# Optimization experiments

Measured on AMD Instinct MI355X. Metric: run time of the kernel, lower is better.

## Reference

```python
import jax, jax.numpy as jnp
import numpy as np

N_NODES = 50000
N_EDGES = 600000
DIN, DH, DOUT = 128, 256, 128
BN_EPS = 1e-5
LRELU_SLOPE = 0.01


def setup_inputs() -> dict:
    key = jax.random.key(0)
    ks = jax.random.split(key, 16)
    rn = lambda k, s, sc=0.05: jax.random.normal(k, s, dtype=jnp.float32) * sc
    return {
        'nodes': jax.random.normal(ks[0], (N_NODES, DIN), dtype=jnp.float32),
        'src': jax.random.randint(ks[1], (N_EDGES,), 0, N_NODES, dtype=jnp.int32),
        'dst': jax.random.randint(ks[2], (N_EDGES,), 0, N_NODES, dtype=jnp.int32),
        # FeedForward params
        'Wf1': rn(ks[3], (DIN, DH)), 'bf1': jnp.zeros((DH,), jnp.float32),
        'gf1': jnp.ones((DH,), jnp.float32), 'bef1': jnp.zeros((DH,), jnp.float32),
        'Wf2': rn(ks[4], (DH, DIN)), 'bf2': jnp.zeros((DIN,), jnp.float32),
        'gf2': jnp.ones((DIN,), jnp.float32), 'bef2': jnp.zeros((DIN,), jnp.float32),
        # SAGEConv 1 (in->hidden)
        'Ws1': rn(ks[5], (DIN, DH)), 'Wn1': rn(ks[6], (DIN, DH)), 'b1': jnp.zeros((DH,), jnp.float32),
        'gs1': jnp.ones((DH,), jnp.float32), 'bs1': jnp.zeros((DH,), jnp.float32),
        # SAGEConv 2 (hidden->out)
        'Ws2': rn(ks[7], (DH, DOUT)), 'Wn2': rn(ks[8], (DH, DOUT)), 'b2': jnp.zeros((DOUT,), jnp.float32),
        'gs2': jnp.ones((DOUT,), jnp.float32), 'bs2': jnp.zeros((DOUT,), jnp.float32),
    }


def _bn(x, gamma, beta):
    # BatchNorm1d, training mode: batch stats over node dim, biased variance
    mu = jnp.mean(x, axis=0)
    var = jnp.mean(jnp.square(x - mu), axis=0)
    return (x - mu) * jax.lax.rsqrt(var + BN_EPS) * gamma + beta


def _sage_mean(x, src, dst, Wself, Wneigh, bias):
    # DGL SAGEConv('mean'): out = x@Wself + mean_{src->dst}(x[src])@Wneigh + bias
    n = x.shape[0]
    deg = jax.ops.segment_sum(jnp.ones_like(src, dtype=x.dtype), dst, num_segments=n)
    agg = jax.ops.segment_sum(x[src], dst, num_segments=n)  # [N, d] irregular scatter-add
    h_neigh = agg / jnp.maximum(deg, 1.0)[:, None]
    return x @ Wself + h_neigh @ Wneigh + bias


def reference(nodes, src, dst, Wf1, bf1, gf1, bef1, Wf2, bf2, gf2, bef2,
              Ws1, Wn1, b1, gs1, bs1, Ws2, Wn2, b2, gs2, bs2):
    # FeedForward (dropout=0 -> identity)
    h = jax.nn.relu(_bn(nodes @ Wf1 + bf1, gf1, bef1))
    h = jax.nn.relu(_bn(h @ Wf2 + bf2, gf2, bef2))
    # SAGE layer 1
    h1 = _sage_mean(h, src, dst, Ws1, Wn1, b1)
    h1 = jax.nn.leaky_relu(_bn(h1, gs1, bs1), LRELU_SLOPE)
    # SAGE layer 2
    h2 = _sage_mean(h1, src, dst, Ws2, Wn2, b2)
    return jax.nn.leaky_relu(_bn(h2, gs2, bs2), LRELU_SLOPE)
```

## Files before the change

### kernel.cpp

```cpp
#include <hip/hip_runtime.h>

#define DIN 128
#define BN_EPS 1e-5f

typedef __attribute__((ext_vector_type(8))) short bf16x8;
typedef __attribute__((ext_vector_type(4))) float f32x4;
typedef unsigned int u32;

__device__ __forceinline__ ushort f2bf(float f) {
    unsigned u = __float_as_uint(f);
    u += 0x7fffu + ((u >> 16) & 1u);
    return (ushort)(u >> 16);
}
__device__ __forceinline__ float bf2f(ushort h) {
    return __uint_as_float(((unsigned)h) << 16);
}

template<int KC, int STATS>
__global__ __launch_bounds__(256) void gemm_wreg(
    const ushort* __restrict__ A, const ushort* __restrict__ BT,
    ushort* __restrict__ C, int mStrips, int N, int K, int logNG,
    float* __restrict__ gsums, float* __restrict__ gsqs)
{
    int tid = threadIdx.x;
    int lane = tid & 63;
    int gw = blockIdx.x * 4 + (tid >> 6);
    int wg = gw & ((1 << logNG) - 1);
    int set = gw >> logNG;
    int totalSets = (gridDim.x * 4) >> logNG;
    int cl = lane & 15, q = lane >> 4;
    int colBase = wg * 64;

    bf16x8 bf[4][KC];
    #pragma unroll
    for (int nt = 0; nt < 4; nt++) {
        const ushort* bp = BT + (long)(colBase + nt * 16 + cl) * K + q * 8;
        #pragma unroll
        for (int kc = 0; kc < KC; kc++)
            bf[nt][kc] = *(const bf16x8*)(bp + kc * 32);
    }

    float ssum[4] = {0.f, 0.f, 0.f, 0.f};
    float ssq[4]  = {0.f, 0.f, 0.f, 0.f};

    for (int strip = set; strip < mStrips; strip += totalSets) {
        int rowBase = strip * 16;
        const ushort* ap = A + (long)(rowBase + cl) * K + q * 8;
        bf16x8 af[KC];
        #pragma unroll
        for (int kc = 0; kc < KC; kc++)
            af[kc] = *(const bf16x8*)(ap + kc * 32);
        f32x4 acc[4] = {};
        #pragma unroll
        for (int kc = 0; kc < KC; kc++)
            #pragma unroll
            for (int nt = 0; nt < 4; nt++)
                acc[nt] = __builtin_amdgcn_mfma_f32_16x16x32_bf16(af[kc], bf[nt][kc], acc[nt], 0, 0, 0);
        #pragma unroll
        for (int nt = 0; nt < 4; nt++) {
            #pragma unroll
            for (int r = 0; r < 4; r++) {
                float v = acc[nt][r];
                long row = rowBase + q * 4 + r;
                C[row * N + colBase + nt * 16 + cl] = f2bf(v);
                if (STATS) { ssum[nt] += v; ssq[nt] += v * v; }
            }
        }
    }

    if (STATS) {
        #pragma unroll
        for (int nt = 0; nt < 4; nt++) {
            ssum[nt] += __shfl_xor(ssum[nt], 16, 64);
            ssum[nt] += __shfl_xor(ssum[nt], 32, 64);
            ssq[nt]  += __shfl_xor(ssq[nt], 16, 64);
            ssq[nt]  += __shfl_xor(ssq[nt], 32, 64);
        }
        if (q == 0) {
            #pragma unroll
            for (int nt = 0; nt < 4; nt++) {
                atomicAdd(&gsums[colBase + nt * 16 + cl], ssum[nt]);
                atomicAdd(&gsqs[colBase + nt * 16 + cl], ssq[nt]);
            }
        }
    }
}

__global__ void bnparam_kernel(const float* __restrict__ sums, const float* __restrict__ sqs,
                               const float* __restrict__ gamma, const float* __restrict__ beta,
                               float* __restrict__ scale, float* __restrict__ shift,
                               int N, float invM)
{
    int c = blockIdx.x * blockDim.x + threadIdx.x;
    if (c < N) {
        float mean = sums[c] * invM;
        float var = sqs[c] * invM - mean * mean;
        float sc = gamma[c] * rsqrtf(var + BN_EPS);
        scale[c] = sc;
        shift[c] = beta[c] - mean * sc;
    }
}

__global__ __launch_bounds__(256) void bnact_bf16(
    const ushort* __restrict__ X, const float* __restrict__ scale, const float* __restrict__ shift,
    ushort* __restrict__ O, int total4, int logN, int outStride, float negSlope)
{
    int stride = gridDim.x * blockDim.x;
    int Nm1 = (1 << logN) - 1;
    for (int t = blockIdx.x * blockDim.x + threadIdx.x; t < total4; t += stride) {
        int idx = t * 4;
        int row = idx >> logN;
        int c = idx & Nm1;
        ushort4 v4 = *(const ushort4*)&X[idx];
        float4 sc = *(const float4*)&scale[c];
        float4 sh = *(const float4*)&shift[c];
        float a = bf2f(v4.x) * sc.x + sh.x; a = (a > 0.f) ? a : a * negSlope;
        float b = bf2f(v4.y) * sc.y + sh.y; b = (b > 0.f) ? b : b * negSlope;
        float d = bf2f(v4.z) * sc.z + sh.z; d = (d > 0.f) ? d : d * negSlope;
        float e = bf2f(v4.w) * sc.w + sh.w; e = (e > 0.f) ? e : e * negSlope;
        ushort4 o; o.x = f2bf(a); o.y = f2bf(b); o.z = f2bf(d); o.w = f2bf(e);
        *(ushort4*)&O[(long)row * outStride + c] = o;
    }
}

__global__ __launch_bounds__(256) void bnact_f32(
    float* __restrict__ X, const float* __restrict__ scale, const float* __restrict__ shift,
    int total4, int logN, float negSlope)
{
    int stride = gridDim.x * blockDim.x;
    int Nm1 = (1 << logN) - 1;
    for (int t = blockIdx.x * blockDim.x + threadIdx.x; t < total4; t += stride) {
        int idx = t * 4;
        int c = idx & Nm1;
        float4 v = *(const float4*)&X[idx];
        float4 sc = *(const float4*)&scale[c];
        float4 sh = *(const float4*)&shift[c];
        float a = v.x * sc.x + sh.x; a = (a > 0.f) ? a : a * negSlope;
        float b = v.y * sc.y + sh.y; b = (b > 0.f) ? b : b * negSlope;
        float d = v.z * sc.z + sh.z; d = (d > 0.f) ? d : d * negSlope;
        float e = v.w * sc.w + sh.w; e = (e > 0.f) ? e : e * negSlope;
        *(float4*)&X[idx] = make_float4(a, b, d, e);
    }
}

__global__ __launch_bounds__(256) void colstats128(
    const float* __restrict__ X, float* __restrict__ sums, float* __restrict__ sqs, int M)
{
    __shared__ float ss[128], sq[128];
    int tid = threadIdx.x;
    if (tid < 128) { ss[tid] = 0.f; sq[tid] = 0.f; }
    __syncthreads();
    int cg = tid & 31;
    int worker = (blockIdx.x << 3) | (tid >> 5);
    int totalW = gridDim.x << 3;
    float4 s4 = make_float4(0, 0, 0, 0), q4 = make_float4(0, 0, 0, 0);
    for (int r = worker; r < M; r += totalW) {
        float4 v = *(const float4*)&X[(long)r * 128 + cg * 4];
        s4.x += v.x; s4.y += v.y; s4.z += v.z; s4.w += v.w;
        q4.x += v.x * v.x; q4.y += v.y * v.y; q4.z += v.z * v.z; q4.w += v.w * v.w;
    }
    atomicAdd(&ss[cg * 4 + 0], s4.x); atomicAdd(&sq[cg * 4 + 0], q4.x);
    atomicAdd(&ss[cg * 4 + 1], s4.y); atomicAdd(&sq[cg * 4 + 1], q4.y);
    atomicAdd(&ss[cg * 4 + 2], s4.z); atomicAdd(&sq[cg * 4 + 2], q4.z);
    atomicAdd(&ss[cg * 4 + 3], s4.w); atomicAdd(&sq[cg * 4 + 3], q4.w);
    __syncthreads();
    if (tid < 128) { atomicAdd(&sums[tid], ss[tid]); atomicAdd(&sqs[tid], sq[tid]); }
}

__global__ void convert_nodes(const float* __restrict__ X, ushort* __restrict__ O, int total4)
{
    int t = blockIdx.x * blockDim.x + threadIdx.x;
    if (t < total4) {
        float4 v = *(const float4*)&X[t * 4];
        ushort4 o; o.x = f2bf(v.x); o.y = f2bf(v.y); o.z = f2bf(v.z); o.w = f2bf(v.w);
        *(ushort4*)&O[t * 4] = o;
    }
}

__global__ void wt_all(const float* __restrict__ W0, const float* __restrict__ W1,
                       const float* __restrict__ W2, const float* __restrict__ W3,
                       const float* __restrict__ W4, const float* __restrict__ W5,
                       ushort* __restrict__ WT)
{
    int seg = blockIdx.y;
    const float* W; int logK, dstBase, stride, kOff;
    switch (seg) {
        case 0: W = W0; logK = 7; dstBase = 0;      stride = 128; kOff = 0;   break;
        case 1: W = W1; logK = 8; dstBase = 32768;  stride = 256; kOff = 0;   break;
        case 2: W = W2; logK = 7; dstBase = 65536;  stride = 256; kOff = 0;   break;
        case 3: W = W3; logK = 7; dstBase = 65536;  stride = 256; kOff = 128; break;
        case 4: W = W4; logK = 8; dstBase = 131072; stride = 256; kOff = 0;   break;
        default:W = W5; logK = 8; dstBase = 163840; stride = 256; kOff = 0;   break;
    }
    int t = blockIdx.x * blockDim.x + threadIdx.x;
    int N = 32768 >> logK;
    int k = t & ((1 << logK) - 1);
    int n = t >> logK;
    WT[(long)dstBase + (long)n * stride + kOff + k] = f2bf(W[(long)k * N + n]);
}

__global__ void degcount_kernel(const int* __restrict__ dst, int* __restrict__ degi, int E)
{
    int i = blockIdx.x * blockDim.x + threadIdx.x;
    if (i < E) atomicAdd(&degi[dst[i]], 1);
}

__global__ __launch_bounds__(256) void scan_block_sums(const int* __restrict__ degi,
                                                       int* __restrict__ partial, int n)
{
    __shared__ int s[256];
    int i = blockIdx.x * 256 + threadIdx.x;
    s[threadIdx.x] = (i < n) ? degi[i] : 0;
    __syncthreads();
    for (int off = 128; off > 0; off >>= 1) {
        if (threadIdx.x < off) s[threadIdx.x] += s[threadIdx.x + off];
        __syncthreads();
    }
    if (threadIdx.x == 0) partial[blockIdx.x] = s[0];
}

__global__ __launch_bounds__(256) void scan_partials(int* __restrict__ partial, int nb)
{
    __shared__ int s[256];
    int v = (threadIdx.x < nb) ? partial[threadIdx.x] : 0;
    s[threadIdx.x] = v;
    __syncthreads();
    for (int off = 1; off < 256; off <<= 1) {
        int t = (threadIdx.x >= off) ? s[threadIdx.x - off] : 0;
        __syncthreads();
        s[threadIdx.x] += t;
        __syncthreads();
    }
    if (threadIdx.x < nb) partial[threadIdx.x] = s[threadIdx.x] - v;
}

__global__ __launch_bounds__(256) void scan_final(const int* __restrict__ degi,
                                                  const int* __restrict__ partial,
                                                  int* __restrict__ rowstart, int n)
{
    __shared__ int s[256];
    int i = blockIdx.x * 256 + threadIdx.x;
    int v = (i < n) ? degi[i] : 0;
    s[threadIdx.x] = v;
    __syncthreads();
    for (int off = 1; off < 256; off <<= 1) {
        int t = (threadIdx.x >= off) ? s[threadIdx.x - off] : 0;
        __syncthreads();
        s[threadIdx.x] += t;
        __syncthreads();
    }
    if (i < n) rowstart[i] = partial[blockIdx.x] + s[threadIdx.x] - v;
}

__global__ void fillcsr_kernel(const int* __restrict__ src, const int* __restrict__ dst,
                               const int* __restrict__ rowstart, int* __restrict__ cursor,
                               int* __restrict__ csr, int E)
{
    int i = blockIdx.x * blockDim.x + threadIdx.x;
    if (i < E) {
        int d = dst[i];
        int p = atomicAdd(&cursor[d], 1);
        csr[rowstart[d] + p] = src[i];
    }
}

__global__ __launch_bounds__(256) void gather_bf(
    const ushort* __restrict__ X, const int* __restrict__ rowstart,
    const int* __restrict__ degi, const int* __restrict__ csr,
    ushort* __restrict__ O, int nN)
{
    int wv = (blockIdx.x * blockDim.x + threadIdx.x) >> 6;
    int lane = threadIdx.x & 63;
    if (wv >= nN) return;
    int start = rowstart[wv], d = degi[wv];
    float a0 = 0.f, a1 = 0.f;
    int col = lane * 2;
    int j = 0;
    for (; j + 4 <= d; j += 4) {
        int s0 = csr[start + j + 0];
        int s1 = csr[start + j + 1];
        int s2 = csr[start + j + 2];
        int s3 = csr[start + j + 3];
        unsigned p0 = *(const unsigned*)(X + (long)s0 * 256 + col);
        unsigned p1 = *(const unsigned*)(X + (long)s1 * 256 + col);
        unsigned p2 = *(const unsigned*)(X + (long)s2 * 256 + col);
        unsigned p3 = *(const unsigned*)(X + (long)s3 * 256 + col);
        a0 += bf2f((ushort)(p0 & 0xffff)) + bf2f((ushort)(p1 & 0xffff))
            + bf2f((ushort)(p2 & 0xffff)) + bf2f((ushort)(p3 & 0xffff));
        a1 += bf2f((ushort)(p0 >> 16)) + bf2f((ushort)(p1 >> 16))
            + bf2f((ushort)(p2 >> 16)) + bf2f((ushort)(p3 >> 16));
    }
    for (; j < d; j++) {
        int s0 = csr[start + j];
        unsigned p0 = *(const unsigned*)(X + (long)s0 * 256 + col);
        a0 += bf2f((ushort)(p0 & 0xffff));
        a1 += bf2f((ushort)(p0 >> 16));
    }
    float inv = 1.f / fmaxf((float)d, 1.f);
    unsigned o = (unsigned)f2bf(a0 * inv) | ((unsigned)f2bf(a1 * inv) << 16);
    *(unsigned*)(O + (long)wv * 256 + col) = o;
}

__global__ __launch_bounds__(256) void gather_fuse(
    const ushort* __restrict__ Z, const int* __restrict__ rowstart,
    const int* __restrict__ degi, const int* __restrict__ csr,
    float* __restrict__ O, int nN)
{
    int wv = (blockIdx.x * blockDim.x + threadIdx.x) >> 6;
    int lane = threadIdx.x & 63;
    if (wv >= nN) return;
    int start = rowstart[wv], d = degi[wv];
    float a0 = 0.f, a1 = 0.f;
    int col = lane * 2;
    int j = 0;
    for (; j + 4 <= d; j += 4) {
        int s0 = csr[start + j + 0];
        int s1 = csr[start + j + 1];
        int s2 = csr[start + j + 2];
        int s3 = csr[start + j + 3];
        unsigned p0 = *(const unsigned*)(Z + (long)s0 * 256 + col);
        unsigned p1 = *(const unsigned*)(Z + (long)s1 * 256 + col);
        unsigned p2 = *(const unsigned*)(Z + (long)s2 * 256 + col);
        unsigned p3 = *(const unsigned*)(Z + (long)s3 * 256 + col);
        a0 += bf2f((ushort)(p0 & 0xffff)) + bf2f((ushort)(p1 & 0xffff))
            + bf2f((ushort)(p2 & 0xffff)) + bf2f((ushort)(p3 & 0xffff));
        a1 += bf2f((ushort)(p0 >> 16)) + bf2f((ushort)(p1 >> 16))
            + bf2f((ushort)(p2 >> 16)) + bf2f((ushort)(p3 >> 16));
    }
    for (; j < d; j++) {
        int s0 = csr[start + j];
        unsigned p0 = *(const unsigned*)(Z + (long)s0 * 256 + col);
        a0 += bf2f((ushort)(p0 & 0xffff));
        a1 += bf2f((ushort)(p0 >> 16));
    }
    float inv = 1.f / fmaxf((float)d, 1.f);
    unsigned sv = *(const unsigned*)(Z + (long)wv * 256 + 128 + col);
    float s0 = bf2f((ushort)(sv & 0xffff));
    float s1 = bf2f((ushort)(sv >> 16));
    *(float2*)(O + (long)wv * 128 + col) = make_float2(a0 * inv + s0, a1 * inv + s1);
}

extern "C" void kernel_launch(void* const* d_in, const int* in_sizes, int n_in,
                              void* d_out, int out_size, void* d_ws, size_t ws_size,
                              hipStream_t stream)
{
    const float* nodes = (const float*)d_in[0];
    const int*   src   = (const int*)d_in[1];
    const int*   dst   = (const int*)d_in[2];
    const float* Wf1   = (const float*)d_in[3];
    const float* gf1   = (const float*)d_in[5];
    const float* bef1  = (const float*)d_in[6];
    const float* Wf2   = (const float*)d_in[7];
    const float* gf2   = (const float*)d_in[9];
    const float* bef2  = (const float*)d_in[10];
    const float* Ws1   = (const float*)d_in[11];
    const float* Wn1   = (const float*)d_in[12];
    const float* gs1   = (const float*)d_in[14];
    const float* bs1   = (const float*)d_in[15];
    const float* Ws2   = (const float*)d_in[16];
    const float* Wn2   = (const float*)d_in[17];
    const float* gs2   = (const float*)d_in[19];
    const float* bs2   = (const float*)d_in[20];

    int nN = in_sizes[0] / DIN;
    int nE = in_sizes[1];
    float* out = (float*)d_out;
    int mStrips = nN / 16;

    ushort* PRE = (ushort*)d_ws;
    ushort* BF1 = PRE + (size_t)nN * 256;
    ushort* BF2 = BF1 + (size_t)nN * 256;
    float* stats = (float*)(BF2 + (size_t)nN * 256);
    float* scale = stats + 2048;
    float* shift = scale + 256;
    ushort* WT   = (ushort*)(shift + 256);
    int* degi     = (int*)(WT + 196608);
    int* cursor   = degi + nN;
    int* rowstart = cursor + nN;
    int* partial  = rowstart + nN;
    int* csr      = partial + 256;

    ushort* Wf1T = WT;
    ushort* Wf2T = WT + 32768;
    ushort* Wc1T = WT + 65536;
    ushort* Wc2T = WT + 131072;

    dim3 blk(256);
    auto cdiv = [](int a, int b) { return (a + b - 1) / b; };
    int nScanBlocks = cdiv(nN, 256);

    convert_nodes<<<dim3(cdiv(nN * DIN / 4, 256)), blk, 0, stream>>>(nodes, BF1, nN * DIN / 4);
    wt_all<<<dim3(128, 6), blk, 0, stream>>>(Wf1, Wf2, Ws1, Wn1, Wn2, Ws2, WT);
    hipMemsetAsync(stats, 0, 2048 * sizeof(float), stream);
    hipMemsetAsync(degi, 0, 2 * (size_t)nN * sizeof(int), stream);

    degcount_kernel<<<dim3(cdiv(nE, 256)), blk, 0, stream>>>(dst, degi, nE);
    scan_block_sums<<<dim3(nScanBlocks), blk, 0, stream>>>(degi, partial, nN);
    scan_partials<<<dim3(1), blk, 0, stream>>>(partial, nScanBlocks);
    scan_final<<<dim3(nScanBlocks), blk, 0, stream>>>(degi, partial, rowstart, nN);
    fillcsr_kernel<<<dim3(cdiv(nE, 256)), blk, 0, stream>>>(src, dst, rowstart, cursor, csr, nE);

    gemm_wreg<4, 1><<<dim3(512), blk, 0, stream>>>(BF1, Wf1T, PRE, mStrips, 256, 128, 2, stats, stats + 256);
    bnparam_kernel<<<dim3(1), blk, 0, stream>>>(stats, stats + 256, gf1, bef1, scale, shift, 256, 1.0f / nN);
    bnact_bf16<<<dim3(2048), blk, 0, stream>>>(PRE, scale, shift, BF1, nN * 256 / 4, 8, 256, 0.0f);

    gemm_wreg<8, 1><<<dim3(256), blk, 0, stream>>>(BF1, Wf2T, PRE, mStrips, 128, 256, 1, stats + 512, stats + 768);
    bnparam_kernel<<<dim3(1), blk, 0, stream>>>(stats + 512, stats + 768, gf2, bef2, scale, shift, 128, 1.0f / nN);
    bnact_bf16<<<dim3(2048), blk, 0, stream>>>(PRE, scale, shift, BF2, nN * 128 / 4, 7, 256, 0.0f);

    gather_bf<<<dim3(cdiv(nN * 64, 256)), blk, 0, stream>>>(BF2, rowstart, degi, csr, BF2 + 128, nN);

    gemm_wreg<8, 1><<<dim3(512), blk, 0, stream>>>(BF2, Wc1T, PRE, mStrips, 256, 256, 2, stats + 1024, stats + 1280);
    bnparam_kernel<<<dim3(1), blk, 0, stream>>>(stats + 1024, stats + 1280, gs1, bs1, scale, shift, 256, 1.0f / nN);
    bnact_bf16<<<dim3(2048), blk, 0, stream>>>(PRE, scale, shift, BF1, nN * 256 / 4, 8, 256, 0.01f);

    gemm_wreg<8, 0><<<dim3(512), blk, 0, stream>>>(BF1, Wc2T, BF2, mStrips, 256, 256, 2, nullptr, nullptr);
    gather_fuse<<<dim3(cdiv(nN * 64, 256)), blk, 0, stream>>>(BF2, rowstart, degi, csr, out, nN);

    colstats128<<<dim3(120), blk, 0, stream>>>(out, stats + 1536, stats + 1792, nN);
    bnparam_kernel<<<dim3(1), blk, 0, stream>>>(stats + 1536, stats + 1792, gs2, bs2, scale, shift, 128, 1.0f / nN);
    bnact_f32<<<dim3(2048), blk, 0, stream>>>(out, scale, shift, nN * 128 / 4, 7, 0.01f);
}
```

Measured before the change: 419.8 us.

## Fuse input conversion and batchnorm activations into GEMM A-operand loads

Removes the separate convert_nodes kernel and the three bnact_bf16 passes. The first GEMM now converts fp32 node features to bf16 while loading them. Later GEMMs and the neighbour gather apply the batchnorm scale, shift and activation to their inputs on the fly, and the workspace is split into PRE1, PRE2, AGG and Z buffers. This saves several full read/write passes over the node activations and a few launches. The cost is extra ALU work inside the GEMM load path, and the gather recomputes the normalization once per edge rather than once per node.

```diff
diff --git a/kernel.cpp b/kernel.cpp
--- a/kernel.cpp
+++ b/kernel.cpp
@@ -3,9 +3,12 @@
 #define DIN 128
 #define BN_EPS 1e-5f
 
+#define AM_CVT    1
+#define AM_BN     2
+#define AM_BNHALF 3
+
 typedef __attribute__((ext_vector_type(8))) short bf16x8;
 typedef __attribute__((ext_vector_type(4))) float f32x4;
-typedef unsigned int u32;
 
 __device__ __forceinline__ ushort f2bf(float f) {
     unsigned u = __float_as_uint(f);
@@ -16,9 +19,12 @@
     return __uint_as_float(((unsigned)h) << 16);
 }
 
-template<int KC, int STATS>
+template<int KC, int STATS, int AMODE>
 __global__ __launch_bounds__(256) void gemm_wreg(
-    const ushort* __restrict__ A, const ushort* __restrict__ BT,
+    const ushort* __restrict__ A, const float* __restrict__ A32,
+    const ushort* __restrict__ A2,
+    const float* __restrict__ bnscale, const float* __restrict__ bnshift, float negSlope,
+    const ushort* __restrict__ BT,
     ushort* __restrict__ C, int mStrips, int N, int K, int logNG,
     float* __restrict__ gsums, float* __restrict__ gsqs)
 {
@@ -45,11 +51,67 @@
 
     for (int strip = set; strip < mStrips; strip += totalSets) {
         int rowBase = strip * 16;
-        const ushort* ap = A + (long)(rowBase + cl) * K + q * 8;
         bf16x8 af[KC];
-        #pragma unroll
-        for (int kc = 0; kc < KC; kc++)
-            af[kc] = *(const bf16x8*)(ap + kc * 32);
+        if (AMODE == AM_CVT) {
+            const float* ap = A32 + (long)(rowBase + cl) * K + q * 8;
+            #pragma unroll
+            for (int kc = 0; kc < KC; kc++) {
+                float4 v0 = *(const float4*)(ap + kc * 32);
+                float4 v1 = *(const float4*)(ap + kc * 32 + 4);
+                ushort* o = (ushort*)&af[kc];
+                o[0] = f2bf(v0.x); o[1] = f2bf(v0.y); o[2] = f2bf(v0.z); o[3] = f2bf(v0.w);
+                o[4] = f2bf(v1.x); o[5] = f2bf(v1.y); o[6] = f2bf(v1.z); o[7] = f2bf(v1.w);
+            }
+        } else if (AMODE == AM_BN) {
+            const ushort* ap = A + (long)(rowBase + cl) * K + q * 8;
+            #pragma unroll
+            for (int kc = 0; kc < KC; kc++) {
+                bf16x8 raw = *(const bf16x8*)(ap + kc * 32);
+                int k0 = kc * 32 + q * 8;
+                float4 s0 = *(const float4*)(bnscale + k0);
+                float4 s1 = *(const float4*)(bnscale + k0 + 4);
+                float4 h0 = *(const float4*)(bnshift + k0);
+                float4 h1 = *(const float4*)(bnshift + k0 + 4);
+                const ushort* r = (const ushort*)&raw;
+                ushort* o = (ushort*)&af[kc];
+                float v;
+                v = bf2f(r[0]) * s0.x + h0.x; v = (v > 0.f) ? v : v * negSlope; o[0] = f2bf(v);
+                v = bf2f(r[1]) * s0.y + h0.y; v = (v > 0.f) ? v : v * negSlope; o[1] = f2bf(v);
+                v = bf2f(r[2]) * s0.z + h0.z; v = (v > 0.f) ? v : v * negSlope; o[2] = f2bf(v);
+                v = bf2f(r[3]) * s0.w + h0.w; v = (v > 0.f) ? v : v * negSlope; o[3] = f2bf(v);
+                v = bf2f(r[4]) * s1.x + h1.x; v = (v > 0.f) ? v : v * negSlope; o[4] = f2bf(v);
+                v = bf2f(r[5]) * s1.y + h1.y; v = (v > 0.f) ? v : v * negSlope; o[5] = f2bf(v);
+                v = bf2f(r[6]) * s1.z + h1.z; v = (v > 0.f) ? v : v * negSlope; o[6] = f2bf(v);
+                v = bf2f(r[7]) * s1.w + h1.w; v = (v > 0.f) ? v : v * negSlope; o[7] = f2bf(v);
+            }
+        } else {
+            const ushort* ap  = A  + (long)(rowBase + cl) * 128 + q * 8;
+            const ushort* ap2 = A2 + (long)(rowBase + cl) * 128 + q * 8;
+            #pragma unroll
+            for (int kc = 0; kc < KC / 2; kc++) {
+                bf16x8 raw = *(const bf16x8*)(ap + kc * 32);
+                int k0 = kc * 32 + q * 8;
+                float4 s0 = *(const float4*)(bnscale + k0);
+                float4 s1 = *(const float4*)(bnscale + k0 + 4);
+                float4 h0 = *(const float4*)(bnshift + k0);
+                float4 h1 = *(const float4*)(bnshift + k0 + 4);
+                const ushort* r = (const ushort*)&raw;
+                ushort* o = (ushort*)&af[kc];
+                float v;
+                v = bf2f(r[0]) * s0.x + h0.x; v = (v > 0.f) ? v : 0.f; o[0] = f2bf(v);
+                v = bf2f(r[1]) * s0.y + h0.y; v = (v > 0.f) ? v : 0.f; o[1] = f2bf(v);
+                v = bf2f(r[2]) * s0.z + h0.z; v = (v > 0.f) ? v : 0.f; o[2] = f2bf(v);
+                v = bf2f(r[3]) * s0.w + h0.w; v = (v > 0.f) ? v : 0.f; o[3] = f2bf(v);
+                v = bf2f(r[4]) * s1.x + h1.x; v = (v > 0.f) ? v : 0.f; o[4] = f2bf(v);
+                v = bf2f(r[5]) * s1.y + h1.y; v = (v > 0.f) ? v : 0.f; o[5] = f2bf(v);
+                v = bf2f(r[6]) * s1.z + h1.z; v = (v > 0.f) ? v : 0.f; o[6] = f2bf(v);
+                v = bf2f(r[7]) * s1.w + h1.w; v = (v > 0.f) ? v : 0.f; o[7] = f2bf(v);
+            }
+            #pragma unroll
+            for (int kc = KC / 2; kc < KC; kc++)
+                af[kc] = *(const bf16x8*)(ap2 + (kc - KC / 2) * 32);
+        }
+
         f32x4 acc[4] = {};
         #pragma unroll
         for (int kc = 0; kc < KC; kc++)
@@ -98,28 +160,6 @@
         float sc = gamma[c] * rsqrtf(var + BN_EPS);
         scale[c] = sc;
         shift[c] = beta[c] - mean * sc;
-    }
-}
-
-__global__ __launch_bounds__(256) void bnact_bf16(
-    const ushort* __restrict__ X, const float* __restrict__ scale, const float* __restrict__ shift,
-    ushort* __restrict__ O, int total4, int logN, int outStride, float negSlope)
-{
-    int stride = gridDim.x * blockDim.x;
-    int Nm1 = (1 << logN) - 1;
-    for (int t = blockIdx.x * blockDim.x + threadIdx.x; t < total4; t += stride) {
-        int idx = t * 4;
-        int row = idx >> logN;
-        int c = idx & Nm1;
-        ushort4 v4 = *(const ushort4*)&X[idx];
-        float4 sc = *(const float4*)&scale[c];
-        float4 sh = *(const float4*)&shift[c];
-        float a = bf2f(v4.x) * sc.x + sh.x; a = (a > 0.f) ? a : a * negSlope;
-        float b = bf2f(v4.y) * sc.y + sh.y; b = (b > 0.f) ? b : b * negSlope;
-        float d = bf2f(v4.z) * sc.z + sh.z; d = (d > 0.f) ? d : d * negSlope;
-        float e = bf2f(v4.w) * sc.w + sh.w; e = (e > 0.f) ? e : e * negSlope;
-        ushort4 o; o.x = f2bf(a); o.y = f2bf(b); o.z = f2bf(d); o.w = f2bf(e);
-        *(ushort4*)&O[(long)row * outStride + c] = o;
     }
 }
 
@@ -167,16 +207,6 @@
     if (tid < 128) { atomicAdd(&sums[tid], ss[tid]); atomicAdd(&sqs[tid], sq[tid]); }
 }
 
-__global__ void convert_nodes(const float* __restrict__ X, ushort* __restrict__ O, int total4)
-{
-    int t = blockIdx.x * blockDim.x + threadIdx.x;
-    if (t < total4) {
-        float4 v = *(const float4*)&X[t * 4];
-        ushort4 o; o.x = f2bf(v.x); o.y = f2bf(v.y); o.z = f2bf(v.z); o.w = f2bf(v.w);
-        *(ushort4*)&O[t * 4] = o;
-    }
-}
-
 __global__ void wt_all(const float* __restrict__ W0, const float* __restrict__ W1,
                        const float* __restrict__ W2, const float* __restrict__ W3,
                        const float* __restrict__ W4, const float* __restrict__ W5,
@@ -264,41 +294,47 @@
     }
 }
 
-__global__ __launch_bounds__(256) void gather_bf(
-    const ushort* __restrict__ X, const int* __restrict__ rowstart,
-    const int* __restrict__ degi, const int* __restrict__ csr,
-    ushort* __restrict__ O, int nN)
+__global__ __launch_bounds__(256) void gather_bn(
+    const ushort* __restrict__ PRE2, const float* __restrict__ scale, const float* __restrict__ shift,
+    const int* __restrict__ rowstart, const int* __restrict__ degi, const int* __restrict__ csr,
+    ushort* __restrict__ AGG, int nN)
 {
     int wv = (blockIdx.x * blockDim.x + threadIdx.x) >> 6;
     int lane = threadIdx.x & 63;
     if (wv >= nN) return;
     int start = rowstart[wv], d = degi[wv];
+    int col = lane * 2;
+    float sc0 = scale[col], sc1 = scale[col + 1];
+    float sh0 = shift[col], sh1 = shift[col + 1];
     float a0 = 0.f, a1 = 0.f;
-    int col = lane * 2;
     int j = 0;
     for (; j + 4 <= d; j += 4) {
         int s0 = csr[start + j + 0];
         int s1 = csr[start + j + 1];
         int s2 = csr[start + j + 2];
         int s3 = csr[start + j + 3];
-        unsigned p0 = *(const unsigned*)(X + (long)s0 * 256 + col);
-        unsigned p1 = *(const unsigned*)(X + (long)s1 * 256 + col);
-        unsigned p2 = *(const unsigned*)(X + (long)s2 * 256 + col);
-        unsigned p3 = *(const unsigned*)(X + (long)s3 * 256 + col);
-        a0 += bf2f((ushort)(p0 & 0xffff)) + bf2f((ushort)(p1 & 0xffff))
-            + bf2f((ushort)(p2 & 0xffff)) + bf2f((ushort)(p3 & 0xffff));
-        a1 += bf2f((ushort)(p0 >> 16)) + bf2f((ushort)(p1 >> 16))
-            + bf2f((ushort)(p2 >> 16)) + bf2f((ushort)(p3 >> 16));
+        unsigned p0 = *(const unsigned*)(PRE2 + (long)s0 * 128 + col);
+        unsigned p1 = *(const unsigned*)(PRE2 + (long)s1 * 128 + col);
+        unsigned p2 = *(const unsigned*)(PRE2 + (long)s2 * 128 + col);
+        unsigned p3 = *(const unsigned*)(PRE2 + (long)s3 * 128 + col);
+        a0 += fmaxf(bf2f((ushort)(p0 & 0xffff)) * sc0 + sh0, 0.f)
+            + fmaxf(bf2f((ushort)(p1 & 0xffff)) * sc0 + sh0, 0.f)
+            + fmaxf(bf2f((ushort)(p2 & 0xffff)) * sc0 + sh0, 0.f)
+            + fmaxf(bf2f((ushort)(p3 & 0xffff)) * sc0 + sh0, 0.f);
+        a1 += fmaxf(bf2f((ushort)(p0 >> 16)) * sc1 + sh1, 0.f)
+            + fmaxf(bf2f((ushort)(p1 >> 16)) * sc1 + sh1, 0.f)
+            + fmaxf(bf2f((ushort)(p2 >> 16)) * sc1 + sh1, 0.f)
+            + fmaxf(bf2f((ushort)(p3 >> 16)) * sc1 + sh1, 0.f);
     }
     for (; j < d; j++) {
         int s0 = csr[start + j];
-        unsigned p0 = *(const unsigned*)(X + (long)s0 * 256 + col);
-        a0 += bf2f((ushort)(p0 & 0xffff));
-        a1 += bf2f((ushort)(p0 >> 16));
+        unsigned p0 = *(const unsigned*)(PRE2 + (long)s0 * 128 + col);
+        a0 += fmaxf(bf2f((ushort)(p0 & 0xffff)) * sc0 + sh0, 0.f);
+        a1 += fmaxf(bf2f((ushort)(p0 >> 16)) * sc1 + sh1, 0.f);
     }
     float inv = 1.f / fmaxf((float)d, 1.f);
     unsigned o = (unsigned)f2bf(a0 * inv) | ((unsigned)f2bf(a1 * inv) << 16);
-    *(unsigned*)(O + (long)wv * 256 + col) = o;
+    *(unsigned*)(AGG + (long)wv * 128 + col) = o;
 }
 
 __global__ __launch_bounds__(256) void gather_fuse(
@@ -366,20 +402,23 @@
     int nE = in_sizes[1];
     float* out = (float*)d_out;
     int mStrips = nN / 16;
-
-    ushort* PRE = (ushort*)d_ws;
-    ushort* BF1 = PRE + (size_t)nN * 256;
-    ushort* BF2 = BF1 + (size_t)nN * 256;
-    float* stats = (float*)(BF2 + (size_t)nN * 256);
-    float* scale = stats + 2048;
-    float* shift = scale + 256;
-    ushort* WT   = (ushort*)(shift + 256);
-    int* degi     = (int*)(WT + 196608);
+    float invM = 1.0f / nN;
+
+    ushort* PRE1 = (ushort*)d_ws;
+    ushort* PRE2 = PRE1 + (size_t)nN * 256;
+    ushort* AGG  = PRE2 + (size_t)nN * 128;
+    ushort* Z    = AGG + (size_t)nN * 128;
+    float* scales = (float*)(Z + (size_t)nN * 256);
+    float* shifts = scales + 4 * 256;
+    float* stats  = shifts + 4 * 256;
+    int* degi     = (int*)(stats + 2048);
     int* cursor   = degi + nN;
     int* rowstart = cursor + nN;
     int* partial  = rowstart + nN;
     int* csr      = partial + 256;
-
+    ushort* WT    = (ushort*)(csr + nE);
+
+    ushort* PRE3 = PRE1;
     ushort* Wf1T = WT;
     ushort* Wf2T = WT + 32768;
     ushort* Wc1T = WT + 65536;
@@ -389,10 +428,8 @@
     auto cdiv = [](int a, int b) { return (a + b - 1) / b; };
     int nScanBlocks = cdiv(nN, 256);
 
-    convert_nodes<<<dim3(cdiv(nN * DIN / 4, 256)), blk, 0, stream>>>(nodes, BF1, nN * DIN / 4);
     wt_all<<<dim3(128, 6), blk, 0, stream>>>(Wf1, Wf2, Ws1, Wn1, Wn2, Ws2, WT);
-    hipMemsetAsync(stats, 0, 2048 * sizeof(float), stream);
-    hipMemsetAsync(degi, 0, 2 * (size_t)nN * sizeof(int), stream);
+    hipMemsetAsync(stats, 0, 2048 * sizeof(float) + 2 * (size_t)nN * sizeof(int), stream);
 
     degcount_kernel<<<dim3(cdiv(nE, 256)), blk, 0, stream>>>(dst, degi, nE);
     scan_block_sums<<<dim3(nScanBlocks), blk, 0, stream>>>(degi, partial, nN);
@@ -400,24 +437,36 @@
     scan_final<<<dim3(nScanBlocks), blk, 0, stream>>>(degi, partial, rowstart, nN);
     fillcsr_kernel<<<dim3(cdiv(nE, 256)), blk, 0, stream>>>(src, dst, rowstart, cursor, csr, nE);
 
-    gemm_wreg<4, 1><<<dim3(512), blk, 0, stream>>>(BF1, Wf1T, PRE, mStrips, 256, 128, 2, stats, stats + 256);
-    bnparam_kernel<<<dim3(1), blk, 0, stream>>>(stats, stats + 256, gf1, bef1, scale, shift, 256, 1.0f / nN);
-    bnact_bf16<<<dim3(2048), blk, 0, stream>>>(PRE, scale, shift, BF1, nN * 256 / 4, 8, 256, 0.0f);
-
-    gemm_wreg<8, 1><<<dim3(256), blk, 0, stream>>>(BF1, Wf2T, PRE, mStrips, 128, 256, 1, stats + 512, stats + 768);
-    bnparam_kernel<<<dim3(1), blk, 0, stream>>>(stats + 512, stats + 768, gf2, bef2, scale, shift, 128, 1.0f / nN);
-    bnact_bf16<<<dim3(2048), blk, 0, stream>>>(PRE, scale, shift, BF2, nN * 128 / 4, 7, 256, 0.0f);
-
-    gather_bf<<<dim3(cdiv(nN * 64, 256)), blk, 0, stream>>>(BF2, rowstart, degi, csr, BF2 + 128, nN);
-
-    gemm_wreg<8, 1><<<dim3(512), blk, 0, stream>>>(BF2, Wc1T, PRE, mStrips, 256, 256, 2, stats + 1024, stats + 1280);
-    bnparam_kernel<<<dim3(1), blk, 0, stream>>>(stats + 1024, stats + 1280, gs1, bs1, scale, shift, 256, 1.0f / nN);
-    bnact_bf16<<<dim3(2048), blk, 0, stream>>>(PRE, scale, shift, BF1, nN * 256 / 4, 8, 256, 0.01f);
-
-    gemm_wreg<8, 0><<<dim3(512), blk, 0, stream>>>(BF1, Wc2T, BF2, mStrips, 256, 256, 2, nullptr, nullptr);
-    gather_fuse<<<dim3(cdiv(nN * 64, 256)), blk, 0, stream>>>(BF2, rowstart, degi, csr, out, nN);
+    gemm_wreg<4, 1, AM_CVT><<<dim3(512), blk, 0, stream>>>(
+        nullptr, nodes, nullptr, nullptr, nullptr, 0.0f,
+        Wf1T, PRE1, mStrips, 256, 128, 2, stats, stats + 256);
+    bnparam_kernel<<<dim3(1), blk, 0, stream>>>(stats, stats + 256, gf1, bef1,
+                                                scales, shifts, 256, invM);
+
+    gemm_wreg<8, 1, AM_BN><<<dim3(256), blk, 0, stream>>>(
+        PRE1, nullptr, nullptr, scales, shifts, 0.0f,
+        Wf2T, PRE2, mStrips, 128, 256, 1, stats + 512, stats + 768);
+    bnparam_kernel<<<dim3(1), blk, 0, stream>>>(stats + 512, stats + 768, gf2, bef2,
+                                                scales + 256, shifts + 256, 128, invM);
+
+    gather_bn<<<dim3(cdiv(nN * 64, 256)), blk, 0, stream>>>(
+        PRE2, scales + 256, shifts + 256, rowstart, degi, csr, AGG, nN);
+
+    gemm_wreg<8, 1, AM_BNHALF><<<dim3(512), blk, 0, stream>>>(
+        PRE2, nullptr, AGG, scales + 256, shifts + 256, 0.0f,
+        Wc1T, PRE3, mStrips, 256, 256, 2, stats + 1024, stats + 1280);
+    bnparam_kernel<<<dim3(1), blk, 0, stream>>>(stats + 1024, stats + 1280, gs1, bs1,
+                                                scales + 512, shifts + 512, 256, invM);
+
+    gemm_wreg<8, 0, AM_BN><<<dim3(512), blk, 0, stream>>>(
+        PRE3, nullptr, nullptr, scales + 512, shifts + 512, 0.01f,
+        Wc2T, Z, mStrips, 256, 256, 2, nullptr, nullptr);
+
+    gather_fuse<<<dim3(cdiv(nN * 64, 256)), blk, 0, stream>>>(Z, rowstart, degi, csr, out, nN);
 
     colstats128<<<dim3(120), blk, 0, stream>>>(out, stats + 1536, stats + 1792, nN);
-    bnparam_kernel<<<dim3(1), blk, 0, stream>>>(stats + 1536, stats + 1792, gs2, bs2, scale, shift, 128, 1.0f / nN);
-    bnact_f32<<<dim3(2048), blk, 0, stream>>>(out, scale, shift, nN * 128 / 4, 7, 0.01f);
-}
+    bnparam_kernel<<<dim3(1), blk, 0, stream>>>(stats + 1536, stats + 1792, gs2, bs2,
+                                                scales + 768, shifts + 768, 128, invM);
+    bnact_f32<<<dim3(2048), blk, 0, stream>>>(out, scales + 768, shifts + 768,
+                                              nN * 128 / 4, 7, 0.01f);
+}
```

Result: no change. 424.7 us (+1.2%).

## Fuse fp32-to-bf16 node conversion into first GEMM and prefetch A strips

Applied to the files above, without the earlier changes.

Removes the separate convert_nodes kernel; the first GEMM now reads fp32 node features directly and converts them to bf16 in registers. The conversion rounds half-up rather than round-to-nearest-even. All GEMMs also gain register double-buffering of the next row strip's A operand, so loads overlap the MFMA and store work. The second GEMM's grid grows from 256 to 512 blocks. This saves a launch and a full write and reread of the bf16 input, at the cost of more registers and possibly lower occupancy.

```diff
diff --git a/kernel.cpp b/kernel.cpp
--- a/kernel.cpp
+++ b/kernel.cpp
@@ -5,7 +5,7 @@
 
 typedef __attribute__((ext_vector_type(8))) short bf16x8;
 typedef __attribute__((ext_vector_type(4))) float f32x4;
-typedef unsigned int u32;
+typedef __attribute__((ext_vector_type(4))) unsigned u32x4;
 
 __device__ __forceinline__ ushort f2bf(float f) {
     unsigned u = __float_as_uint(f);
@@ -16,9 +16,10 @@
     return __uint_as_float(((unsigned)h) << 16);
 }
 
-template<int KC, int STATS>
+template<int KC, int STATS, int CVT>
 __global__ __launch_bounds__(256) void gemm_wreg(
-    const ushort* __restrict__ A, const ushort* __restrict__ BT,
+    const ushort* __restrict__ A, const float* __restrict__ A32,
+    const ushort* __restrict__ BT,
     ushort* __restrict__ C, int mStrips, int N, int K, int logNG,
     float* __restrict__ gsums, float* __restrict__ gsqs)
 {
@@ -43,28 +44,91 @@
     float ssum[4] = {0.f, 0.f, 0.f, 0.f};
     float ssq[4]  = {0.f, 0.f, 0.f, 0.f};
 
-    for (int strip = set; strip < mStrips; strip += totalSets) {
-        int rowBase = strip * 16;
-        const ushort* ap = A + (long)(rowBase + cl) * K + q * 8;
-        bf16x8 af[KC];
-        #pragma unroll
-        for (int kc = 0; kc < KC; kc++)
-            af[kc] = *(const bf16x8*)(ap + kc * 32);
-        f32x4 acc[4] = {};
-        #pragma unroll
-        for (int kc = 0; kc < KC; kc++)
+    bf16x8 curH[KC], nxtH[KC];
+    u32x4 curF[CVT ? 2 * KC : 1], nxtF[CVT ? 2 * KC : 1];
+
+    int strip = set;
+    if (strip < mStrips) {
+        if (CVT) {
+            const unsigned* ap = (const unsigned*)(A32 + (long)(strip * 16 + cl) * K + q * 8);
             #pragma unroll
-            for (int nt = 0; nt < 4; nt++)
-                acc[nt] = __builtin_amdgcn_mfma_f32_16x16x32_bf16(af[kc], bf[nt][kc], acc[nt], 0, 0, 0);
-        #pragma unroll
-        for (int nt = 0; nt < 4; nt++) {
+            for (int kc = 0; kc < KC; kc++) {
+                curF[2 * kc + 0] = *(const u32x4*)(ap + kc * 32);
+                curF[2 * kc + 1] = *(const u32x4*)(ap + kc * 32 + 4);
+            }
+        } else {
+            const ushort* ap = A + (long)(strip * 16 + cl) * K + q * 8;
             #pragma unroll
-            for (int r = 0; r < 4; r++) {
-                float v = acc[nt][r];
-                long row = rowBase + q * 4 + r;
-                C[row * N + colBase + nt * 16 + cl] = f2bf(v);
-                if (STATS) { ssum[nt] += v; ssq[nt] += v * v; }
-            }
+            for (int kc = 0; kc < KC; kc++)
+                curH[kc] = *(const bf16x8*)(ap + kc * 32);
+        }
+
+        for (;;) {
+            int next = strip + totalSets;
+            bool has = next < mStrips;
+            if (has) {
+                if (CVT) {
+                    const unsigned* ap = (const unsigned*)(A32 + (long)(next * 16 + cl) * K + q * 8);
+                    #pragma unroll
+                    for (int kc = 0; kc < KC; kc++) {
+                        nxtF[2 * kc + 0] = *(const u32x4*)(ap + kc * 32);
+                        nxtF[2 * kc + 1] = *(const u32x4*)(ap + kc * 32 + 4);
+                    }
+                } else {
+                    const ushort* ap = A + (long)(next * 16 + cl) * K + q * 8;
+                    #pragma unroll
+                    for (int kc = 0; kc < KC; kc++)
+                        nxtH[kc] = *(const bf16x8*)(ap + kc * 32);
+                }
+            }
+
+            bf16x8 af[KC];
+            if (CVT) {
+                #pragma unroll
+                for (int kc = 0; kc < KC; kc++) {
+                    unsigned* o = (unsigned*)&af[kc];
+                    #pragma unroll
+                    for (int p = 0; p < 2; p++) {
+                        u32x4 r = curF[2 * kc + p];
+                        unsigned a0 = r[0] + 0x8000u, a1 = r[1] + 0x8000u;
+                        unsigned a2 = r[2] + 0x8000u, a3 = r[3] + 0x8000u;
+                        o[2 * p + 0] = (a0 >> 16) | (a1 & 0xffff0000u);
+                        o[2 * p + 1] = (a2 >> 16) | (a3 & 0xffff0000u);
+                    }
+                }
+            } else {
+                #pragma unroll
+                for (int kc = 0; kc < KC; kc++) af[kc] = curH[kc];
+            }
+
+            f32x4 acc[4] = {};
+            #pragma unroll
+            for (int kc = 0; kc < KC; kc++)
+                #pragma unroll
+                for (int nt = 0; nt < 4; nt++)
+                    acc[nt] = __builtin_amdgcn_mfma_f32_16x16x32_bf16(af[kc], bf[nt][kc], acc[nt], 0, 0, 0);
+
+            int rowBase = strip * 16;
+            #pragma unroll
+            for (int nt = 0; nt < 4; nt++) {
+                #pragma unroll
+                for (int r = 0; r < 4; r++) {
+                    float v = acc[nt][r];
+                    long row = rowBase + q * 4 + r;
+                    C[row * N + colBase + nt * 16 + cl] = f2bf(v);
+                    if (STATS) { ssum[nt] += v; ssq[nt] += v * v; }
+                }
+            }
+
+            if (!has) break;
+            if (CVT) {
+                #pragma unroll
+                for (int i = 0; i < 2 * KC; i++) curF[i] = nxtF[i];
+            } else {
+                #pragma unroll
+                for (int kc = 0; kc < KC; kc++) curH[kc] = nxtH[kc];
+            }
+            strip = next;
         }
     }
 
@@ -165,16 +229,6 @@
     atomicAdd(&ss[cg * 4 + 3], s4.w); atomicAdd(&sq[cg * 4 + 3], q4.w);
     __syncthreads();
     if (tid < 128) { atomicAdd(&sums[tid], ss[tid]); atomicAdd(&sqs[tid], sq[tid]); }
-}
-
-__global__ void convert_nodes(const float* __restrict__ X, ushort* __restrict__ O, int total4)
-{
-    int t = blockIdx.x * blockDim.x + threadIdx.x;
-    if (t < total4) {
-        float4 v = *(const float4*)&X[t * 4];
-        ushort4 o; o.x = f2bf(v.x); o.y = f2bf(v.y); o.z = f2bf(v.z); o.w = f2bf(v.w);
-        *(ushort4*)&O[t * 4] = o;
-    }
 }
 
 __global__ void wt_all(const float* __restrict__ W0, const float* __restrict__ W1,
@@ -389,7 +443,6 @@
     auto cdiv = [](int a, int b) { return (a + b - 1) / b; };
     int nScanBlocks = cdiv(nN, 256);
 
-    convert_nodes<<<dim3(cdiv(nN * DIN / 4, 256)), blk, 0, stream>>>(nodes, BF1, nN * DIN / 4);
     wt_all<<<dim3(128, 6), blk, 0, stream>>>(Wf1, Wf2, Ws1, Wn1, Wn2, Ws2, WT);
     hipMemsetAsync(stats, 0, 2048 * sizeof(float), stream);
     hipMemsetAsync(degi, 0, 2 * (size_t)nN * sizeof(int), stream);
@@ -400,21 +453,25 @@
     scan_final<<<dim3(nScanBlocks), blk, 0, stream>>>(degi, partial, rowstart, nN);
     fillcsr_kernel<<<dim3(cdiv(nE, 256)), blk, 0, stream>>>(src, dst, rowstart, cursor, csr, nE);
 
-    gemm_wreg<4, 1><<<dim3(512), blk, 0, stream>>>(BF1, Wf1T, PRE, mStrips, 256, 128, 2, stats, stats + 256);
+    gemm_wreg<4, 1, 1><<<dim3(512), blk, 0, stream>>>(
+        nullptr, nodes, Wf1T, PRE, mStrips, 256, 128, 2, stats, stats + 256);
     bnparam_kernel<<<dim3(1), blk, 0, stream>>>(stats, stats + 256, gf1, bef1, scale, shift, 256, 1.0f / nN);
     bnact_bf16<<<dim3(2048), blk, 0, stream>>>(PRE, scale, shift, BF1, nN * 256 / 4, 8, 256, 0.0f);
 
-    gemm_wreg<8, 1><<<dim3(256), blk, 0, stream>>>(BF1, Wf2T, PRE, mStrips, 128, 256, 1, stats + 512, stats + 768);
+    gemm_wreg<8, 1, 0><<<dim3(512), blk, 0, stream>>>(
+        BF1, nullptr, Wf2T, PRE, mStrips, 128, 256, 1, stats + 512, stats + 768);
     bnparam_kernel<<<dim3(1), blk, 0, stream>>>(stats + 512, stats + 768, gf2, bef2, scale, shift, 128, 1.0f / nN);
     bnact_bf16<<<dim3(2048), blk, 0, stream>>>(PRE, scale, shift, BF2, nN * 128 / 4, 7, 256, 0.0f);
 
     gather_bf<<<dim3(cdiv(nN * 64, 256)), blk, 0, stream>>>(BF2, rowstart, degi, csr, BF2 + 128, nN);
 
-    gemm_wreg<8, 1><<<dim3(512), blk, 0, stream>>>(BF2, Wc1T, PRE, mStrips, 256, 256, 2, stats + 1024, stats + 1280);
+    gemm_wreg<8, 1, 0><<<dim3(512), blk, 0, stream>>>(
+        BF2, nullptr, Wc1T, PRE, mStrips, 256, 256, 2, stats + 1024, stats + 1280);
     bnparam_kernel<<<dim3(1), blk, 0, stream>>>(stats + 1024, stats + 1280, gs1, bs1, scale, shift, 256, 1.0f / nN);
     bnact_bf16<<<dim3(2048), blk, 0, stream>>>(PRE, scale, shift, BF1, nN * 256 / 4, 8, 256, 0.01f);
 
-    gemm_wreg<8, 0><<<dim3(512), blk, 0, stream>>>(BF1, Wc2T, BF2, mStrips, 256, 256, 2, nullptr, nullptr);
+    gemm_wreg<8, 0, 0><<<dim3(512), blk, 0, stream>>>(
+        BF1, nullptr, Wc2T, BF2, mStrips, 256, 256, 2, nullptr, nullptr);
     gather_fuse<<<dim3(cdiv(nN * 64, 256)), blk, 0, stream>>>(BF2, rowstart, degi, csr, out, nN);
 
     colstats128<<<dim3(120), blk, 0, stream>>>(out, stats + 1536, stats + 1792, nN);
```

After: 431.7 us. +2.8%, slower.
